# Performance work log

Hardware: AMD Instinct MI355X
Metric: run time of the kernel (lower is better)

## Reference

```python
import jax, jax.numpy as jnp
import numpy as np
import math

D_MODEL = 1024
N_HEADS = 16
HEAD_DIM = 64
BATCH = 2
SEQ = 2048


def setup_inputs() -> dict:
    key = jax.random.key(0)
    ks = jax.random.split(key, 5)
    x = jax.random.normal(ks[0], (BATCH, SEQ, D_MODEL), dtype=jnp.float32)
    s = 0.02
    wq = jax.random.normal(ks[1], (D_MODEL, D_MODEL), dtype=jnp.float32) * s
    wk = jax.random.normal(ks[2], (D_MODEL, D_MODEL), dtype=jnp.float32) * s
    wv = jax.random.normal(ks[3], (D_MODEL, D_MODEL), dtype=jnp.float32) * s
    wo = jax.random.normal(ks[4], (D_MODEL, D_MODEL), dtype=jnp.float32) * s
    gammas = jnp.linspace(0.9, 0.99, N_HEADS, dtype=jnp.float32)
    return {"x": x, "wq": wq, "wk": wk, "wv": wv, "wo": wo, "gammas": gammas}


def _decay_mask(length: int, gammas: jnp.ndarray, dtype) -> jnp.ndarray:
    # [H, L, L]: gamma^(t-s) for t >= s, else 0 (causal exponential decay)
    pos = jnp.arange(length)
    diff = pos[:, None] - pos[None, :]
    causal = diff >= 0
    d = jnp.maximum(diff, 0).astype(dtype)
    g = gammas.astype(dtype)[:, None, None]
    return jnp.where(causal[None], jnp.power(g, d[None]), jnp.zeros((), dtype))


def reference(x, wq, wk, wv, wo, gammas):
    B, L, D = x.shape
    H, hd = N_HEADS, HEAD_DIM
    # torch nn.Linear: y = x @ W.T
    q = (x @ wq.T).reshape(B, L, H, hd)
    k = (x @ wk.T).reshape(B, L, H, hd)
    v = (x @ wv.T).reshape(B, L, H, hd)
    scale = 1.0 / math.sqrt(hd)
    scores = jnp.einsum('bthd,bshd->bhts', q * scale, k)  # [B,H,L,L]
    decay = _decay_mask(L, gammas, x.dtype)               # [H,L,L]
    weights = scores * decay[None]
    retained = jnp.einsum('bhts,bshd->bthd', weights, v)  # [B,L,H,hd]
    return retained.reshape(B, L, H * hd) @ wo.T
```

## Files before the change

### kernel.cpp

```cpp
#include <hip/hip_runtime.h>


typedef __attribute__((ext_vector_type(8))) short bf16x8;
typedef __attribute__((ext_vector_type(4))) float f32x4;
typedef __attribute__((ext_vector_type(16))) float f32x16;
typedef __attribute__((ext_vector_type(4))) unsigned short u16x4;
typedef __attribute__((ext_vector_type(8))) unsigned short u16x8;
typedef __attribute__((ext_vector_type(4))) unsigned int u32x4;

__device__ inline unsigned short f2bf(float f) {
    unsigned int u;
    __builtin_memcpy(&u, &f, 4);
    u += 0x7fffu + ((u >> 16) & 1u);
    return (unsigned short)(u >> 16);
}

__device__ inline f32x4 mfma16(bf16x8 a, bf16x8 b, f32x4 c) {
    return __builtin_amdgcn_mfma_f32_16x16x32_bf16(a, b, c, 0, 0, 0);
}
__device__ inline f32x16 mfma32(bf16x8 a, bf16x8 b, f32x16 c) {
    return __builtin_amdgcn_mfma_f32_32x32x16_bf16(a, b, c, 0, 0, 0);
}

__device__ inline void gl16(const unsigned short* g, unsigned short* l) {
    __builtin_amdgcn_global_load_lds(
        (const __attribute__((address_space(1))) unsigned int*)g,
        (__attribute__((address_space(3))) unsigned int*)l,
        16, 0, 0);
}

__device__ inline unsigned cvtpk(float lo, float hi) {
    unsigned r;
    asm("v_cvt_pk_bf16_f32 %0, %1, %2" : "=v"(r) : "v"(lo), "v"(hi));
    return r;
}

__global__ __launch_bounds__(256) void convert_bf16(
    const float* __restrict__ x,
    const float* __restrict__ wq, const float* __restrict__ wk,
    const float* __restrict__ wv, const float* __restrict__ wo,
    unsigned short* __restrict__ xb,
    unsigned short* __restrict__ wqb, unsigned short* __restrict__ wkb,
    unsigned short* __restrict__ wvb, unsigned short* __restrict__ wob)
{
    int cid = blockIdx.x * 256 + threadIdx.x;
    #pragma unroll
    for (int it = 0; it < 4; ++it, cid += 262144) {
        const float* src;
        unsigned short* dst;
        size_t off;
        if (cid < 524288) {
            src = x; dst = xb; off = (size_t)cid * 8;
        } else {
            const int t = cid - 524288;
            const int seg = t >> 17;
            off = (size_t)(t & 131071) * 8;
            src = seg == 0 ? wq : seg == 1 ? wk : seg == 2 ? wv : wo;
            dst = seg == 0 ? wqb : seg == 1 ? wkb : seg == 2 ? wvb : wob;
        }
        f32x4 a = *(const f32x4*)(src + off);
        f32x4 b = *(const f32x4*)(src + off + 4);
        u32x4 v = { cvtpk(a[0], a[1]), cvtpk(a[2], a[3]),
                    cvtpk(b[0], b[1]), cvtpk(b[2], b[3]) };
        *(u32x4*)(dst + off) = v;
    }
}

__global__ __launch_bounds__(256) void qkv_bf16(
    const unsigned short* __restrict__ xb,
    const unsigned short* __restrict__ wqb, const unsigned short* __restrict__ wkb,
    const unsigned short* __restrict__ wvb,
    unsigned short* __restrict__ qfr, unsigned short* __restrict__ kfr,
    unsigned short* __restrict__ vfr)
{
    __shared__ unsigned short sR[128 * 64];
    __shared__ unsigned short sL[128 * 64];

    const int z = blockIdx.z;
    const unsigned short* W = (z == 0) ? wqb : (z == 1) ? wkb : wvb;
    const unsigned short* Rs = (z < 2) ? xb : W;
    const unsigned short* Ls = (z < 2) ? W : xb;
    const int rblk = (z < 2) ? blockIdx.x : blockIdx.y;
    const int lblk = (z < 2) ? blockIdx.y : blockIdx.x;

    const int tid = threadIdx.x;
    const int l = tid & 63, w = tid >> 6;
    const int lrow = l & 15, koff4 = (l >> 4) * 4;
    const int swz = lrow & 7;
    const int wrow = (w >> 1) * 64, wcol = (w & 1) * 64;

    f32x4 acc[4][4] = {};

    const int srow = w * 32 + (l >> 3);
    const int scol = ((l & 7) ^ ((l >> 3) & 7)) * 8;
    const unsigned short* gR = Rs + (size_t)(rblk * 128 + srow) * 1024 + scol;
    const unsigned short* gL = Ls + (size_t)(lblk * 128 + srow) * 1024 + scol;
    unsigned short* lRb = sR + (w * 32) * 64;
    unsigned short* lLb = sL + (w * 32) * 64;

    auto stage = [&](int kk) {
        #pragma unroll
        for (int p = 0; p < 4; ++p) {
            gl16(gR + (size_t)p * 8 * 1024 + kk, lRb + p * 512);
            gl16(gL + (size_t)p * 8 * 1024 + kk, lLb + p * 512);
        }
    };

    stage(0);
    for (int kk = 0; kk < 1024; kk += 64) {
        asm volatile("s_waitcnt vmcnt(0)" ::: "memory");
        __builtin_amdgcn_s_barrier();
        __builtin_amdgcn_sched_barrier(0);

        bf16x8 aL[2][4], bR[2][4];
        #pragma unroll
        for (int kt = 0; kt < 2; ++kt)
            #pragma unroll
            for (int f = 0; f < 4; ++f) {
                const int co = ((kt * 4 + (l >> 4)) ^ swz) * 8;
                aL[kt][f] = *(const bf16x8*)&sL[(wcol + f * 16 + lrow) * 64 + co];
                bR[kt][f] = *(const bf16x8*)&sR[(wrow + f * 16 + lrow) * 64 + co];
            }
        asm volatile("s_waitcnt lgkmcnt(0)" ::: "memory");
        __builtin_amdgcn_sched_barrier(0);
        __builtin_amdgcn_s_barrier();
        __builtin_amdgcn_sched_barrier(0);

        if (kk + 64 < 1024) stage(kk + 64);

        __builtin_amdgcn_s_setprio(1);
        #pragma unroll
        for (int kt = 0; kt < 2; ++kt)
            #pragma unroll
            for (int af = 0; af < 4; ++af)
                #pragma unroll
                for (int bf = 0; bf < 4; ++bf)
                    acc[af][bf] = mfma16(aL[kt][af], bR[kt][bf], acc[af][bf]);
        __builtin_amdgcn_s_setprio(0);
    }

    #pragma unroll
    for (int af = 0; af < 4; ++af) {
        #pragma unroll
        for (int bf = 0; bf < 4; ++bf) {
            const int m = rblk * 128 + wrow + bf * 16 + lrow;
            const int n0 = lblk * 128 + wcol + af * 16 + koff4;
            f32x4 v = acc[af][bf];
            unsigned p0 = cvtpk(v[0], v[1]), p1 = cvtpk(v[2], v[3]);
            u16x4 val = { (unsigned short)(p0 & 0xffff), (unsigned short)(p0 >> 16),
                          (unsigned short)(p1 & 0xffff), (unsigned short)(p1 >> 16) };
            if (z < 2) {
                const int bq = m >> 11, s = m & 2047;
                const int h2 = n0 >> 6, dd = n0 & 63;
                const size_t addr = (size_t)((bq * 16 + h2) * 64 + (s >> 5)) * 2048
                                  + (size_t)(dd >> 4) * 512 + (size_t)((dd >> 3) & 1) * 256
                                  + (size_t)(s & 31) * 8 + (dd & 7);
                unsigned short* dst = z ? kfr : qfr;
                *(u16x4*)(dst + addr) = val;
            } else {
                const int h2 = m >> 6, dd = m & 63;
                const int bq = n0 >> 11, t = n0 & 2047;
                const size_t addr = (size_t)((bq * 16 + h2) * 64 + (t >> 5)) * 2048
                                  + (size_t)((dd >> 5) * 2 + ((t >> 4) & 1)) * 512
                                  + (size_t)((t >> 3) & 1) * 256
                                  + (size_t)(dd & 31) * 8 + (t & 7);
                *(u16x4*)(vfr + addr) = val;
            }
        }
    }
}

__global__ __launch_bounds__(256) void retention_lds(
    const unsigned short* __restrict__ qfr, const unsigned short* __restrict__ kfr,
    const unsigned short* __restrict__ vfr, const float* __restrict__ gammas,
    unsigned short* __restrict__ ret)
{
    __shared__ unsigned short kv[4][2][4096];

    const int bid = blockIdx.x;
    const int xcd = bid & 7;
    const int r_ = bid >> 3;
    const int p = r_ >> 2;
    const int m = ((r_ & 3) + (r_ >> 5)) & 3;
    const int tw = 63 - p;
    const int b = m >> 1;
    const int pi = b ? (7 - xcd) : xcd;
    const int h = (m & 1) ? (15 - pi) : pi;
    const float lg = log2f(gammas[h]);
    const int cut_i = (int)(45.0f / (-lg));
    const float gi32 = exp2f(-32.0f * lg);

    const int tid = threadIdx.x;
    const int l = tid & 63, w = tid >> 6;
    const int l31 = l & 31, hi = l >> 5;
    const int tw0 = tw << 5;
    const int tq = tw0 + l31;

    const size_t hbase = (size_t)((b * 16 + h) * 64) * 2048;
    const unsigned short* qfb = qfr + hbase + l * 8;
    const unsigned short* kfb = kfr + hbase + l * 8;
    const unsigned short* vfb = vfr + hbase + l * 8;

    bf16x8 qf[4];
    #pragma unroll
    for (int kt = 0; kt < 4; ++kt)
        qf[kt] = *(const bf16x8*)(qfb + (size_t)tw * 2048 + kt * 512);

    float cf[16];
    #pragma unroll
    for (int r = 0; r < 16; ++r) {
        const int crow = (r & 3) + (hi << 2) + ((r >> 2) << 3);
        cf[r] = exp2f((float)(31 - crow) * lg);
    }

    int sb_lo = tw0 - 31 - cut_i;
    sb_lo = (sb_lo <= 0) ? 0 : (sb_lo >> 5);

    const int n = tw - sb_lo + 1;
    const int chunk = (n + 3) >> 2;
    const int my_lo = sb_lo + w * chunk;
    int my_hi = my_lo + chunk;
    if (my_hi > tw + 1) my_hi = tw + 1;

    unsigned short* slot[2] = { &kv[w][0][0], &kv[w][1][0] };

    auto stage = [&](int sb, unsigned short* s) {
        const unsigned short* kp = kfb + (size_t)sb * 2048;
        const unsigned short* vp = vfb + (size_t)sb * 2048;
        #pragma unroll
        for (int t = 0; t < 4; ++t) gl16(kp + t * 512, s + t * 512);
        #pragma unroll
        for (int t = 0; t < 4; ++t) gl16(vp + t * 512, s + 2048 + t * 512);
    };

    f32x16 acc0 = {}, acc1 = {};

    if (my_lo < my_hi) {
        float rowf = 0.125f * exp2f((float)(tq - (my_lo << 5) - 31) * lg);
        stage(my_lo, slot[0]);
        if (my_lo + 1 < my_hi) stage(my_lo + 1, slot[1]);

        for (int sb = my_lo; sb < my_hi; ++sb) {
            unsigned short* cur = slot[(sb - my_lo) & 1];
            if (sb + 1 < my_hi) asm volatile("s_waitcnt vmcnt(8)" ::: "memory");
            else                asm volatile("s_waitcnt vmcnt(0)" ::: "memory");
            __builtin_amdgcn_sched_barrier(0);

            bf16x8 kc[4], vc[4];
            #pragma unroll
            for (int kt = 0; kt < 4; ++kt)
                kc[kt] = *(const bf16x8*)(cur + kt * 512 + l * 8);
            #pragma unroll
            for (int i = 0; i < 4; ++i)
                vc[i] = *(const bf16x8*)(cur + 2048 + i * 512 + l * 8);

            f32x16 sc = {};
            __builtin_amdgcn_s_setprio(1);
            #pragma unroll
            for (int kt = 0; kt < 4; ++kt) sc = mfma32(kc[kt], qf[kt], sc);
            __builtin_amdgcn_s_setprio(0);

            float wv_[16];
            if (sb == tw) {
                const int dtq = tq - (sb << 5);
                #pragma unroll
                for (int r = 0; r < 16; ++r) {
                    const int crow = (r & 3) + (hi << 2) + ((r >> 2) << 3);
                    float t_ = sc[r] * rowf * cf[r];
                    wv_[r] = (dtq >= crow) ? t_ : 0.0f;
                }
            } else {
                #pragma unroll
                for (int r = 0; r < 16; ++r)
                    wv_[r] = sc[r] * rowf * cf[r];
            }
            unsigned pk_[8];
            #pragma unroll
            for (int i = 0; i < 8; ++i) pk_[i] = cvtpk(wv_[2 * i], wv_[2 * i + 1]);
            asm("v_permlane32_swap_b32 %0, %1" : "+v"(pk_[0]), "+v"(pk_[2]));
            asm("v_permlane32_swap_b32 %0, %1" : "+v"(pk_[1]), "+v"(pk_[3]));
            asm("v_permlane32_swap_b32 %0, %1" : "+v"(pk_[4]), "+v"(pk_[6]));
            asm("v_permlane32_swap_b32 %0, %1" : "+v"(pk_[5]), "+v"(pk_[7]));
            u32x4 f0v = { pk_[0], pk_[1], pk_[2], pk_[3] };
            u32x4 f1v = { pk_[4], pk_[5], pk_[6], pk_[7] };
            const bf16x8 pa0 = __builtin_bit_cast(bf16x8, f0v);
            const bf16x8 pa1 = __builtin_bit_cast(bf16x8, f1v);
            __builtin_amdgcn_s_setprio(1);
            acc0 = mfma32(pa0, vc[0], acc0);
            acc0 = mfma32(pa1, vc[1], acc0);
            acc1 = mfma32(pa0, vc[2], acc1);
            acc1 = mfma32(pa1, vc[3], acc1);
            __builtin_amdgcn_s_setprio(0);
            rowf *= gi32;

            if (sb + 2 < my_hi) {
                asm volatile("s_waitcnt lgkmcnt(0)" ::: "memory");
                __builtin_amdgcn_sched_barrier(0);
                stage(sb + 2, cur);
            }
        }
    }

    __syncthreads();
    float* red = (float*)&kv[0][0][0];
    if (w > 0) {
        #pragma unroll
        for (int r = 0; r < 16; ++r) {
            red[(w - 1) * 2048 + r * 64 + l]        = acc0[r];
            red[(w - 1) * 2048 + (r + 16) * 64 + l] = acc1[r];
        }
    }
    __syncthreads();
    if (w == 0) {
        #pragma unroll
        for (int jj = 0; jj < 3; ++jj)
            #pragma unroll
            for (int r = 0; r < 16; ++r) {
                acc0[r] += red[jj * 2048 + r * 64 + l];
                acc1[r] += red[jj * 2048 + (r + 16) * 64 + l];
            }
        #pragma unroll
        for (int r = 0; r < 16; ++r) {
            const int tl = (r & 3) + (hi << 2) + ((r >> 2) << 3);
            unsigned short* dst = ret + (size_t)(b * 2048 + tw0 + tl) * 1024 + h * 64 + l31;
            dst[0]  = f2bf(acc0[r]);
            dst[32] = f2bf(acc1[r]);
        }
    }
}

__global__ __launch_bounds__(256) void out_bf16(
    const unsigned short* __restrict__ ret, const unsigned short* __restrict__ wob,
    float* __restrict__ out)
{
    __shared__ unsigned short sR[128 * 64];
    __shared__ unsigned short sL[128 * 64];

    const int rblk = blockIdx.x;
    const int lblk = blockIdx.y;

    const int tid = threadIdx.x;
    const int l = tid & 63, w = tid >> 6;
    const int lrow = l & 15, koff4 = (l >> 4) * 4;
    const int swz = lrow & 7;
    const int wrow = (w >> 1) * 64, wcol = (w & 1) * 64;

    f32x4 acc[4][4] = {};

    const int srow = w * 32 + (l >> 3);
    const int scol = ((l & 7) ^ ((l >> 3) & 7)) * 8;
    const unsigned short* gR = ret + (size_t)(rblk * 128 + srow) * 1024 + scol;
    const unsigned short* gL = wob + (size_t)(lblk * 128 + srow) * 1024 + scol;
    unsigned short* lRb = sR + (w * 32) * 64;
    unsigned short* lLb = sL + (w * 32) * 64;

    auto stage = [&](int kk) {
        #pragma unroll
        for (int p = 0; p < 4; ++p) {
            gl16(gR + (size_t)p * 8 * 1024 + kk, lRb + p * 512);
            gl16(gL + (size_t)p * 8 * 1024 + kk, lLb + p * 512);
        }
    };

    stage(0);
    for (int kk = 0; kk < 1024; kk += 64) {
        asm volatile("s_waitcnt vmcnt(0)" ::: "memory");
        __builtin_amdgcn_s_barrier();
        __builtin_amdgcn_sched_barrier(0);

        bf16x8 aL[2][4], bR[2][4];
        #pragma unroll
        for (int kt = 0; kt < 2; ++kt)
            #pragma unroll
            for (int f = 0; f < 4; ++f) {
                const int co = ((kt * 4 + (l >> 4)) ^ swz) * 8;
                aL[kt][f] = *(const bf16x8*)&sL[(wcol + f * 16 + lrow) * 64 + co];
                bR[kt][f] = *(const bf16x8*)&sR[(wrow + f * 16 + lrow) * 64 + co];
            }
        asm volatile("s_waitcnt lgkmcnt(0)" ::: "memory");
        __builtin_amdgcn_sched_barrier(0);
        __builtin_amdgcn_s_barrier();
        __builtin_amdgcn_sched_barrier(0);

        if (kk + 64 < 1024) stage(kk + 64);

        __builtin_amdgcn_s_setprio(1);
        #pragma unroll
        for (int kt = 0; kt < 2; ++kt)
            #pragma unroll
            for (int af = 0; af < 4; ++af)
                #pragma unroll
                for (int bf = 0; bf < 4; ++bf)
                    acc[af][bf] = mfma16(aL[kt][af], bR[kt][bf], acc[af][bf]);
        __builtin_amdgcn_s_setprio(0);
    }

    #pragma unroll
    for (int af = 0; af < 4; ++af)
        #pragma unroll
        for (int bf = 0; bf < 4; ++bf) {
            const int m = rblk * 128 + wrow + bf * 16 + lrow;
            const int n0 = lblk * 128 + wcol + af * 16 + koff4;
            *(f32x4*)(out + (size_t)m * 1024 + n0) = acc[af][bf];
        }
}

extern "C" void kernel_launch(void* const* d_in, const int* in_sizes, int n_in,
                              void* d_out, int out_size, void* d_ws, size_t ws_size,
                              hipStream_t stream) {
    const float* x      = (const float*)d_in[0];
    const float* wq     = (const float*)d_in[1];
    const float* wk     = (const float*)d_in[2];
    const float* wv     = (const float*)d_in[3];
    const float* wo     = (const float*)d_in[4];
    const float* gammas = (const float*)d_in[5];
    float* out = (float*)d_out;

    unsigned short* ws = (unsigned short*)d_ws;
    unsigned short* qf  = ws;
    unsigned short* kf  = ws + (size_t)4 * 1024 * 1024;
    unsigned short* vf  = ws + (size_t)8 * 1024 * 1024;
    unsigned short* ret = ws + (size_t)12 * 1024 * 1024;
    unsigned short* xb  = ret;
    unsigned short* wqb = ws + (size_t)16 * 1024 * 1024;
    unsigned short* wkb = ws + (size_t)17 * 1024 * 1024;
    unsigned short* wvb = ws + (size_t)18 * 1024 * 1024;
    unsigned short* wob = ws + (size_t)19 * 1024 * 1024;

    convert_bf16<<<1024, 256, 0, stream>>>(x, wq, wk, wv, wo, xb, wqb, wkb, wvb, wob);
    qkv_bf16<<<dim3(32, 8, 3), 256, 0, stream>>>(xb, wqb, wkb, wvb, qf, kf, vf);
    retention_lds<<<2048, 256, 0, stream>>>(qf, kf, vf, gammas, ret);
    out_bf16<<<dim3(32, 8), 256, 0, stream>>>(ret, wob, out);
}
```

Before: 92.11 us.

## Share K/V tiles across four query tiles per block in retention kernel

Reworks the retention kernel so each block handles four consecutive query tiles (one per wave) and the waves share a single double-buffered K/V stage in LDS, each wave loading a quarter of each tile. Before, each block handled one query tile and split its key range across waves, which needed a cross-wave reduction at the end. The aim is to cut global K/V traffic roughly fourfold and drop the reduction, at the cost of two block barriers per key tile, a 4x smaller grid (512 blocks), and less parallelism per query tile. Row decay factors are now recomputed with exp2 on every iteration instead of updated by multiplication.

```diff
diff --git a/kernel.cpp b/kernel.cpp
--- a/kernel.cpp
+++ b/kernel.cpp
@@ -170,29 +170,29 @@
     }
 }
 
-__global__ __launch_bounds__(256) void retention_lds(
+__global__ __launch_bounds__(256) void retention_shared(
     const unsigned short* __restrict__ qfr, const unsigned short* __restrict__ kfr,
     const unsigned short* __restrict__ vfr, const float* __restrict__ gammas,
     unsigned short* __restrict__ ret)
 {
-    __shared__ unsigned short kv[4][2][4096];
+    __shared__ unsigned short kv[2][4096];
 
     const int bid = blockIdx.x;
     const int xcd = bid & 7;
-    const int r_ = bid >> 3;
-    const int p = r_ >> 2;
-    const int m = ((r_ & 3) + (r_ >> 5)) & 3;
-    const int tw = 63 - p;
+    const int j = bid >> 3;
+    const int m = j & 3;
+    const int pp = 15 - (j >> 2);
     const int b = m >> 1;
     const int pi = b ? (7 - xcd) : xcd;
     const int h = (m & 1) ? (15 - pi) : pi;
     const float lg = log2f(gammas[h]);
     const int cut_i = (int)(45.0f / (-lg));
-    const float gi32 = exp2f(-32.0f * lg);
 
     const int tid = threadIdx.x;
     const int l = tid & 63, w = tid >> 6;
     const int l31 = l & 31, hi = l >> 5;
+    const int tw = pp * 4 + w;
+    const int twB = pp * 4 + 3;
     const int tw0 = tw << 5;
     const int tq = tw0 + l31;
 
@@ -213,61 +213,60 @@
         cf[r] = exp2f((float)(31 - crow) * lg);
     }
 
-    int sb_lo = tw0 - 31 - cut_i;
-    sb_lo = (sb_lo <= 0) ? 0 : (sb_lo >> 5);
-
-    const int n = tw - sb_lo + 1;
-    const int chunk = (n + 3) >> 2;
-    const int my_lo = sb_lo + w * chunk;
-    int my_hi = my_lo + chunk;
-    if (my_hi > tw + 1) my_hi = tw + 1;
-
-    unsigned short* slot[2] = { &kv[w][0][0], &kv[w][1][0] };
-
-    auto stage = [&](int sb, unsigned short* s) {
-        const unsigned short* kp = kfb + (size_t)sb * 2048;
-        const unsigned short* vp = vfb + (size_t)sb * 2048;
-        #pragma unroll
-        for (int t = 0; t < 4; ++t) gl16(kp + t * 512, s + t * 512);
-        #pragma unroll
-        for (int t = 0; t < 4; ++t) gl16(vp + t * 512, s + 2048 + t * 512);
+    int lo = ((pp * 4) << 5) - 31 - cut_i;
+    lo = (lo <= 0) ? 0 : (lo >> 5);
+
+    auto stage = [&](int sb, int bufi) {
+        const unsigned short* kp = kfb + (size_t)sb * 2048 + w * 512;
+        const unsigned short* vp = vfb + (size_t)sb * 2048 + w * 512;
+        unsigned short* s = &kv[bufi][0];
+        gl16(kp, s + w * 512);
+        gl16(vp, s + 2048 + w * 512);
     };
 
     f32x16 acc0 = {}, acc1 = {};
 
-    if (my_lo < my_hi) {
-        float rowf = 0.125f * exp2f((float)(tq - (my_lo << 5) - 31) * lg);
-        stage(my_lo, slot[0]);
-        if (my_lo + 1 < my_hi) stage(my_lo + 1, slot[1]);
-
-        for (int sb = my_lo; sb < my_hi; ++sb) {
-            unsigned short* cur = slot[(sb - my_lo) & 1];
-            if (sb + 1 < my_hi) asm volatile("s_waitcnt vmcnt(8)" ::: "memory");
-            else                asm volatile("s_waitcnt vmcnt(0)" ::: "memory");
-            __builtin_amdgcn_sched_barrier(0);
-
-            bf16x8 kc[4], vc[4];
-            #pragma unroll
-            for (int kt = 0; kt < 4; ++kt)
-                kc[kt] = *(const bf16x8*)(cur + kt * 512 + l * 8);
-            #pragma unroll
-            for (int i = 0; i < 4; ++i)
-                vc[i] = *(const bf16x8*)(cur + 2048 + i * 512 + l * 8);
-
+    stage(lo, 0);
+    if (lo + 1 <= twB) stage(lo + 1, 1);
+
+    for (int sb = lo; sb <= twB; ++sb) {
+        const int cur = (sb - lo) & 1;
+        if (sb < twB) asm volatile("s_waitcnt vmcnt(2)" ::: "memory");
+        else          asm volatile("s_waitcnt vmcnt(0)" ::: "memory");
+        __builtin_amdgcn_sched_barrier(0);
+        __builtin_amdgcn_s_barrier();
+        __builtin_amdgcn_sched_barrier(0);
+
+        bf16x8 kc[4], vc[4];
+        const unsigned short* kvc = &kv[cur][0];
+        #pragma unroll
+        for (int kt = 0; kt < 4; ++kt)
+            kc[kt] = *(const bf16x8*)(kvc + kt * 512 + l * 8);
+        #pragma unroll
+        for (int i = 0; i < 4; ++i)
+            vc[i] = *(const bf16x8*)(kvc + 2048 + i * 512 + l * 8);
+        asm volatile("s_waitcnt lgkmcnt(0)" ::: "memory");
+        __builtin_amdgcn_sched_barrier(0);
+        __builtin_amdgcn_s_barrier();
+        __builtin_amdgcn_sched_barrier(0);
+
+        if (sb + 2 <= twB) stage(sb + 2, cur);
+
+        if (sb <= tw) {
             f32x16 sc = {};
             __builtin_amdgcn_s_setprio(1);
             #pragma unroll
             for (int kt = 0; kt < 4; ++kt) sc = mfma32(kc[kt], qf[kt], sc);
             __builtin_amdgcn_s_setprio(0);
 
+            const float rowf = 0.125f * exp2f((float)(tq - (sb << 5) - 31) * lg);
             float wv_[16];
             if (sb == tw) {
-                const int dtq = tq - (sb << 5);
                 #pragma unroll
                 for (int r = 0; r < 16; ++r) {
                     const int crow = (r & 3) + (hi << 2) + ((r >> 2) << 3);
                     float t_ = sc[r] * rowf * cf[r];
-                    wv_[r] = (dtq >= crow) ? t_ : 0.0f;
+                    wv_[r] = (l31 >= crow) ? t_ : 0.0f;
                 }
             } else {
                 #pragma unroll
@@ -291,41 +290,15 @@
             acc1 = mfma32(pa0, vc[2], acc1);
             acc1 = mfma32(pa1, vc[3], acc1);
             __builtin_amdgcn_s_setprio(0);
-            rowf *= gi32;
-
-            if (sb + 2 < my_hi) {
-                asm volatile("s_waitcnt lgkmcnt(0)" ::: "memory");
-                __builtin_amdgcn_sched_barrier(0);
-                stage(sb + 2, cur);
-            }
-        }
-    }
-
-    __syncthreads();
-    float* red = (float*)&kv[0][0][0];
-    if (w > 0) {
-        #pragma unroll
-        for (int r = 0; r < 16; ++r) {
-            red[(w - 1) * 2048 + r * 64 + l]        = acc0[r];
-            red[(w - 1) * 2048 + (r + 16) * 64 + l] = acc1[r];
-        }
-    }
-    __syncthreads();
-    if (w == 0) {
-        #pragma unroll
-        for (int jj = 0; jj < 3; ++jj)
-            #pragma unroll
-            for (int r = 0; r < 16; ++r) {
-                acc0[r] += red[jj * 2048 + r * 64 + l];
-                acc1[r] += red[jj * 2048 + (r + 16) * 64 + l];
-            }
-        #pragma unroll
-        for (int r = 0; r < 16; ++r) {
-            const int tl = (r & 3) + (hi << 2) + ((r >> 2) << 3);
-            unsigned short* dst = ret + (size_t)(b * 2048 + tw0 + tl) * 1024 + h * 64 + l31;
-            dst[0]  = f2bf(acc0[r]);
-            dst[32] = f2bf(acc1[r]);
-        }
+        }
+    }
+
+    #pragma unroll
+    for (int r = 0; r < 16; ++r) {
+        const int tl = (r & 3) + (hi << 2) + ((r >> 2) << 3);
+        unsigned short* dst = ret + (size_t)(b * 2048 + tw0 + tl) * 1024 + h * 64 + l31;
+        dst[0]  = f2bf(acc0[r]);
+        dst[32] = f2bf(acc1[r]);
     }
 }
 
@@ -429,6 +402,6 @@
 
     convert_bf16<<<1024, 256, 0, stream>>>(x, wq, wk, wv, wo, xb, wqb, wkb, wvb, wob);
     qkv_bf16<<<dim3(32, 8, 3), 256, 0, stream>>>(xb, wqb, wkb, wvb, qf, kf, vf);
-    retention_lds<<<2048, 256, 0, stream>>>(qf, kf, vf, gammas, ret);
+    retention_shared<<<512, 256, 0, stream>>>(qf, kf, vf, gammas, ret);
     out_bf16<<<dim3(32, 8), 256, 0, stream>>>(ret, wob, out);
 }
```

Measured after the change: 96.21 us. 4.5% more time.
